# Kernel optimization log

Measured on AMD Instinct MI355X. Metric: run time of the kernel, lower is better.

## Reference

```python
import jax, jax.numpy as jnp
import numpy as np

B, T, D, K = 8, 4096, 1024, 3


def setup_inputs() -> dict:
    key = jax.random.key(0)
    k0, k1, k2 = jax.random.split(key, 3)
    x = jax.random.normal(k0, (B, T, D), dtype=jnp.float32)
    lim = 1.0 / np.sqrt(D)
    Wv = jax.random.uniform(k1, (D, D), dtype=jnp.float32, minval=-lim, maxval=lim)
    bv = jnp.zeros((D,), dtype=jnp.float32)
    Wo = jax.random.uniform(k2, (D, D), dtype=jnp.float32, minval=-lim, maxval=lim)
    bo = jnp.zeros((D,), dtype=jnp.float32)
    neighbor_weights = jnp.ones((K,), dtype=jnp.float32) / K
    return {"x": x, "Wv": Wv, "bv": bv, "Wo": Wo, "bo": bo,
            "neighbor_weights": neighbor_weights}


def reference(x, Wv, bv, Wo, bo, neighbor_weights):
    # x: [B, T, D]; faithful translation of the unfold -> Linear -> weighted-sum chain
    k = neighbor_weights.shape[0]
    pad = k // 2
    t = x.shape[1]
    # replicate padding along T (torch F.pad mode='replicate')
    xp = jnp.pad(x, ((0, 0), (pad, pad), (0, 0)), mode='edge')  # [B, T+2*pad, D]
    # sliding windows: [B, T, K, D] (small fixed K loop, not a data-dim loop)
    windows = jnp.stack([xp[:, i:i + t, :] for i in range(k)], axis=2)
    # value projection applied per window element (nn.Linear: x @ W.T + b)
    v = jnp.einsum('btkd,ed->btke', windows, Wv) + bv  # [B, T, K, D]
    # fixed-weight neighbor average
    attended = jnp.einsum('btkd,k->btd', v, neighbor_weights)  # [B, T, D]
    # output projection
    return jnp.einsum('btd,ed->bte', attended, Wo) + bo
```

## Files before the change

kernel.cpp:

```cpp
#include <hip/hip_runtime.h>
#include <stdint.h>
#include <stddef.h>

typedef _Float16 f16_t;
typedef _Float16 f16x4 __attribute__((ext_vector_type(4)));
typedef _Float16 f16x8 __attribute__((ext_vector_type(8)));
typedef float f32x4 __attribute__((ext_vector_type(4)));

#define AS_G __attribute__((address_space(1)))
#define AS_L __attribute__((address_space(3)))

__device__ __forceinline__ void gload_lds16(const void* g, void* l) {
  __builtin_amdgcn_global_load_lds((AS_G void*)g, (AS_L void*)l, 16, 0, 0);
}

#define FENCE() asm volatile("" ::: "memory")
#define BARX()                            \
  do {                                    \
    FENCE();                              \
    __builtin_amdgcn_s_barrier();         \
    FENCE();                              \
  } while (0)
#define VMCNT(n) asm volatile("s_waitcnt vmcnt(" #n ")" ::: "memory")


__global__ void cvt_f16_kernel(const float* __restrict__ in, f16_t* __restrict__ out, int n4) {
  int i = blockIdx.x * blockDim.x + threadIdx.x;
  if (i >= n4) return;
  f32x4 v = ((const f32x4*)in)[i];
  f16x4 o;
  o.x = (f16_t)v.x; o.y = (f16_t)v.y; o.z = (f16_t)v.z; o.w = (f16_t)v.w;
  ((f16x4*)out)[i] = o;
}

__global__ void transpose_cvt_kernel(const float* __restrict__ in, f16_t* __restrict__ out) {
  __shared__ float tile[32][33];
  const int bx = blockIdx.x, by = blockIdx.y;
  const int tx = threadIdx.x, ty = threadIdx.y;
#pragma unroll
  for (int i = 0; i < 32; i += 8)
    tile[ty + i][tx] = in[(size_t)(by * 32 + ty + i) * 1024 + bx * 32 + tx];
  __syncthreads();
#pragma unroll
  for (int i = 0; i < 32; i += 8)
    out[(size_t)(bx * 32 + ty + i) * 1024 + by * 32 + tx] = (f16_t)tile[tx][ty + i];
}

__global__ void bconst_kernel(const float* __restrict__ Wo, const float* __restrict__ bv,
                              const float* __restrict__ bo, const float* __restrict__ nw,
                              int Kw, float* __restrict__ bc) {
  const int e = blockIdx.x;
  const int t = threadIdx.x;
  float sw = 0.f;
  for (int k = 0; k < Kw; ++k) sw += nw[k];
  float p = 0.f;
  for (int d = t; d < 1024; d += 256) p += Wo[(size_t)e * 1024 + d] * bv[d];
  __shared__ float red[256];
  red[t] = p;
  __syncthreads();
  for (int s = 128; s > 0; s >>= 1) {
    if (t < s) red[t] += red[t + s];
    __syncthreads();
  }
  if (t == 0) bc[e] = sw * red[0] + bo[e];
}

__global__ void xavg_kernel(const float* __restrict__ x, const float* __restrict__ nw,
                            f16_t* __restrict__ out) {
  const int T = 4096, D = 1024;
  const int base = blockIdx.x * 8;
  const int t0 = base & (T - 1);
  const int col = threadIdx.x * 4;
  const float w0 = nw[0], w1 = nw[1], w2 = nw[2];
  const float* xb = x + (size_t)base * D + col;
  f32x4 a = *(const f32x4*)(xb + (t0 == 0 ? 0 : -D));
  f32x4 b = *(const f32x4*)(xb);
  f16_t* ob = out + (size_t)base * D + col;
#pragma unroll
  for (int g = 0; g < 8; ++g) {
    f32x4 c;
    if (t0 + g == T - 1) c = b;
    else c = *(const f32x4*)(xb + (size_t)(g + 1) * D);
    f32x4 y = w0 * a + w1 * b + w2 * c;
    f16x4 o;
    o.x = (f16_t)y.x; o.y = (f16_t)y.y; o.z = (f16_t)y.z; o.w = (f16_t)y.w;
    *(f16x4*)(ob + (size_t)g * D) = o;
    a = b;
    b = c;
  }
}


template <typename OutT, bool BIAS>
__global__ __launch_bounds__(256) void gemm_bt_kernel(const f16_t* __restrict__ A,
                                                      const f16_t* __restrict__ Bt,
                                                      OutT* __restrict__ C,
                                                      const float* __restrict__ bias,
                                                      int M, int N, int K) {
  __shared__ __align__(16) f16_t sA[128 * 32];
  __shared__ __align__(16) f16_t sB[128 * 32];
  const int tid = threadIdx.x;
  const int l = tid & 63;
  const int w = tid >> 6;
  const int wr = w >> 1;
  const int wc = w & 1;
  const int nMT = M >> 7;
  const int bid = blockIdx.x;
  const int mt = bid % nMT;
  const int nt = bid / nMT;
  const int m0 = mt << 7;
  const int n0 = nt << 7;

  const int srow = (w << 4) + (l >> 2);
  const int scol = (l & 3) << 3;
  const size_t aoff0 = (size_t)(m0 + srow) * K + scol;
  const size_t boff0 = (size_t)(n0 + srow) * K + scol;
  f16_t* ldsA = sA + (w << 9);
  f16_t* ldsB = sB + (w << 9);

  f32x4 acc[4][4];
#pragma unroll
  for (int i = 0; i < 4; ++i)
#pragma unroll
    for (int j = 0; j < 4; ++j) acc[i][j] = f32x4{0.f, 0.f, 0.f, 0.f};

  const int ka = (l >> 4) << 3;
  const int ar = (wr << 6) + (l & 15);
  const int br = (wc << 6) + (l & 15);

  const int nK = K >> 5;
  for (int kt = 0; kt < nK; ++kt) {
    const int kb = kt << 5;
    gload_lds16(A + aoff0 + kb, ldsA);
    gload_lds16(A + aoff0 + ((size_t)K << 6) + kb, ldsA + 2048);
    gload_lds16(Bt + boff0 + kb, ldsB);
    gload_lds16(Bt + boff0 + ((size_t)K << 6) + kb, ldsB + 2048);
    __syncthreads();
    f16x8 af[4], bfr[4];
#pragma unroll
    for (int m = 0; m < 4; ++m) af[m] = *(const f16x8*)(sA + ((ar + (m << 4)) << 5) + ka);
#pragma unroll
    for (int n = 0; n < 4; ++n) bfr[n] = *(const f16x8*)(sB + ((br + (n << 4)) << 5) + ka);
#pragma unroll
    for (int m = 0; m < 4; ++m)
#pragma unroll
      for (int n = 0; n < 4; ++n)
        acc[m][n] = __builtin_amdgcn_mfma_f32_16x16x32_f16(af[m], bfr[n], acc[m][n], 0, 0, 0);
    __syncthreads();
  }

  const int orow = (l >> 4) << 2;
  const int ocol = l & 15;
#pragma unroll
  for (int n = 0; n < 4; ++n) {
    const int gn = n0 + (wc << 6) + (n << 4) + ocol;
    const float bs = BIAS ? bias[gn] : 0.f;
#pragma unroll
    for (int m = 0; m < 4; ++m) {
      const int gm = m0 + (wr << 6) + (m << 4) + orow;
#pragma unroll
      for (int j = 0; j < 4; ++j) {
        C[(size_t)(gm + j) * N + gn] = (OutT)(acc[m][n][j] + bs);
      }
    }
  }
}


__device__ __forceinline__ void stage256(const f16_t* __restrict__ g, int K,
                                         f16_t* ldsOp, int w, int l) {
#pragma unroll
  for (int i = 0; i < 2; ++i) {
    const int f = i * 512 + w * 64 + l;
    const int row = f >> 2;
    const int ch = f & 3;
    const int col = ((ch ^ ((row >> 1) & 3)) << 3);
    gload_lds16(g + (size_t)row * K + col, ldsOp + i * 4096 + w * 512);
  }
}

__global__ __launch_bounds__(512, 2) void gemm256_kernel(const f16_t* __restrict__ A,
                                                         const f16_t* __restrict__ Bt,
                                                         float* __restrict__ C,
                                                         const float* __restrict__ bias,
                                                         int M, int N, int K) {
  __shared__ __align__(16) f16_t lds[4 * 16384];
  const int tid = threadIdx.x;
  const int l = tid & 63;
  const int w = tid >> 6;
  const int wr = w >> 2;
  const int wc = w & 3;

  const int nwg = gridDim.x;
  const int cpx = nwg >> 3;
  const int swz = (blockIdx.x & 7) * cpx + (blockIdx.x >> 3);
  const int nNT = N >> 8;
  const int mt = swz / nNT;
  const int nt = swz % nNT;
  const int m0 = mt << 8;
  const int n0 = nt << 8;

  const f16_t* Apanel = A + (size_t)m0 * K;
  const f16_t* Bpanel = Bt + (size_t)n0 * K;

  const int lr = l & 15;
  const int q = l >> 4;
  const int sw = ((q ^ ((lr >> 1) & 3)) << 3);

  f32x4 acc[8][4];
#pragma unroll
  for (int m = 0; m < 8; ++m)
#pragma unroll
    for (int n = 0; n < 4; ++n) acc[m][n] = f32x4{0.f, 0.f, 0.f, 0.f};

  const int nK = K >> 5;

  for (int t = 0; t < 3; ++t) {
    f16_t* buf = lds + (t & 3) * 16384;
    stage256(Apanel + (t << 5), K, buf, w, l);
    stage256(Bpanel + (t << 5), K, buf + 8192, w, l);
  }
  VMCNT(8);
  BARX();

  for (int t = 0; t < nK; ++t) {
    f16_t* sA = lds + (t & 3) * 16384;
    f16_t* sB = sA + 8192;

    f16x8 bf[4], af[4];
#pragma unroll
    for (int n = 0; n < 4; ++n)
      bf[n] = *(const f16x8*)(sB + (((wc << 6) + (n << 4) + lr) << 5) + sw);
#pragma unroll
    for (int m = 0; m < 4; ++m)
      af[m] = *(const f16x8*)(sA + (((wr << 7) + (m << 4) + lr) << 5) + sw);
    if (t + 3 < nK) {
      f16_t* nbuf = lds + ((t + 3) & 3) * 16384;
      stage256(Apanel + ((size_t)(t + 3) << 5), K, nbuf, w, l);
    }
    BARX();
    __builtin_amdgcn_s_setprio(1);
#pragma unroll
    for (int m = 0; m < 4; ++m)
#pragma unroll
      for (int n = 0; n < 4; ++n)
        acc[m][n] = __builtin_amdgcn_mfma_f32_16x16x32_f16(af[m], bf[n], acc[m][n], 0, 0, 0);
    __builtin_amdgcn_s_setprio(0);
    BARX();

    f16x8 ag[4];
#pragma unroll
    for (int m = 0; m < 4; ++m)
      ag[m] = *(const f16x8*)(sA + (((wr << 7) + 64 + (m << 4) + lr) << 5) + sw);
    if (t + 3 < nK) {
      f16_t* nbuf = lds + ((t + 3) & 3) * 16384;
      stage256(Bpanel + ((size_t)(t + 3) << 5), K, nbuf + 8192, w, l);
    }
    BARX();
    __builtin_amdgcn_s_setprio(1);
#pragma unroll
    for (int m = 0; m < 4; ++m)
#pragma unroll
      for (int n = 0; n < 4; ++n)
        acc[m + 4][n] = __builtin_amdgcn_mfma_f32_16x16x32_f16(ag[m], bf[n], acc[m + 4][n], 0, 0, 0);
    __builtin_amdgcn_s_setprio(0);
    VMCNT(8);
    BARX();
  }

  float bs[4];
#pragma unroll
  for (int n = 0; n < 4; ++n) bs[n] = bias[n0 + (wc << 6) + (n << 4) + lr];
#pragma unroll
  for (int m = 0; m < 8; ++m) {
    const int gm = m0 + (wr << 7) + (m << 4) + (q << 2);
#pragma unroll
    for (int j = 0; j < 4; ++j) {
      float* Crow = C + (size_t)(gm + j) * N + n0 + (wc << 6) + lr;
#pragma unroll
      for (int n = 0; n < 4; ++n) Crow[n << 4] = acc[m][n][j] + bs[n];
    }
  }
}


extern "C" void kernel_launch(void* const* d_in, const int* in_sizes, int n_in,
                              void* d_out, int out_size, void* d_ws, size_t ws_size,
                              hipStream_t stream) {
  const float* x = (const float*)d_in[0];
  const float* Wv = (const float*)d_in[1];
  const float* bv = (const float*)d_in[2];
  const float* Wo = (const float*)d_in[3];
  const float* bo = (const float*)d_in[4];
  const float* nw = (const float*)d_in[5];
  float* out = (float*)d_out;

  char* ws = (char*)d_ws;
  f16_t* Wo_h = (f16_t*)(ws);
  f16_t* WvT  = (f16_t*)(ws + (2u << 20));
  f16_t* WcT  = (f16_t*)(ws + (4u << 20));
  float* bc   = (float*)(ws + (6u << 20));
  f16_t* Xavg = (f16_t*)(ws + (8u << 20));

  cvt_f16_kernel<<<dim3(1024), dim3(256), 0, stream>>>(Wo, Wo_h, 1024 * 1024 / 4);
  transpose_cvt_kernel<<<dim3(32, 32), dim3(32, 8), 0, stream>>>(Wv, WvT);
  bconst_kernel<<<dim3(1024), dim3(256), 0, stream>>>(Wo, bv, bo, nw, in_sizes[5], bc);
  xavg_kernel<<<dim3(32768 / 8), dim3(256), 0, stream>>>(x, nw, Xavg);
  gemm_bt_kernel<f16_t, false><<<dim3(64), dim3(256), 0, stream>>>(
      Wo_h, WvT, WcT, (const float*)nullptr, 1024, 1024, 1024);
  gemm256_kernel<<<dim3(512), dim3(512), 0, stream>>>(
      Xavg, WcT, out, bc, 32768, 1024, 1024);
}
```

Baseline: 158.7 us.

## Fuse neighbor-averaging of x into the main GEMM A-tile loading

Removes the separate xavg kernel that wrote an averaged fp16 copy of x, and instead loads fp32 x rows directly in the main GEMM, computes the 3-tap weighted average in registers, converts to fp16 and writes it into a padded LDS A tile. B staging becomes a 3-stage ring while A is double-buffered through registers. The intent is to avoid the 64MB fp16 intermediate write and read-back. In exchange the GEMM reads fp32 x with roughly 2x row redundancy (4 rows per 2 outputs) through plain vector loads, and the pipeline depth for A shrinks.

Measured after the change: 155.2 us. 1.02x faster.

```diff
diff --git a/kernel.cpp b/kernel.cpp
--- a/kernel.cpp
+++ b/kernel.cpp
@@ -22,6 +22,7 @@
     FENCE();                              \
   } while (0)
 #define VMCNT(n) asm volatile("s_waitcnt vmcnt(" #n ")" ::: "memory")
+#define LGKM0() asm volatile("s_waitcnt lgkmcnt(0)" ::: "memory")
 
 
 __global__ void cvt_f16_kernel(const float* __restrict__ in, f16_t* __restrict__ out, int n4) {
@@ -63,31 +64,6 @@
     __syncthreads();
   }
   if (t == 0) bc[e] = sw * red[0] + bo[e];
-}
-
-__global__ void xavg_kernel(const float* __restrict__ x, const float* __restrict__ nw,
-                            f16_t* __restrict__ out) {
-  const int T = 4096, D = 1024;
-  const int base = blockIdx.x * 8;
-  const int t0 = base & (T - 1);
-  const int col = threadIdx.x * 4;
-  const float w0 = nw[0], w1 = nw[1], w2 = nw[2];
-  const float* xb = x + (size_t)base * D + col;
-  f32x4 a = *(const f32x4*)(xb + (t0 == 0 ? 0 : -D));
-  f32x4 b = *(const f32x4*)(xb);
-  f16_t* ob = out + (size_t)base * D + col;
-#pragma unroll
-  for (int g = 0; g < 8; ++g) {
-    f32x4 c;
-    if (t0 + g == T - 1) c = b;
-    else c = *(const f32x4*)(xb + (size_t)(g + 1) * D);
-    f32x4 y = w0 * a + w1 * b + w2 * c;
-    f16x4 o;
-    o.x = (f16_t)y.x; o.y = (f16_t)y.y; o.z = (f16_t)y.z; o.w = (f16_t)y.w;
-    *(f16x4*)(ob + (size_t)g * D) = o;
-    a = b;
-    b = c;
-  }
 }
 
 
@@ -167,8 +143,8 @@
 }
 
 
-__device__ __forceinline__ void stage256(const f16_t* __restrict__ g, int K,
-                                         f16_t* ldsOp, int w, int l) {
+__device__ __forceinline__ void stageB(const f16_t* __restrict__ g, int K,
+                                       f16_t* ldsOp, int w, int l) {
 #pragma unroll
   for (int i = 0; i < 2; ++i) {
     const int f = i * 512 + w * 64 + l;
@@ -179,33 +155,77 @@
   }
 }
 
-__global__ __launch_bounds__(512, 2) void gemm256_kernel(const f16_t* __restrict__ A,
-                                                         const f16_t* __restrict__ Bt,
-                                                         float* __restrict__ C,
-                                                         const float* __restrict__ bias,
-                                                         int M, int N, int K) {
-  __shared__ __align__(16) f16_t lds[4 * 16384];
+__global__ __launch_bounds__(512, 2) void gemm_fused_kernel(
+    const float* __restrict__ X, const f16_t* __restrict__ Bt,
+    float* __restrict__ C, const float* __restrict__ bias,
+    const float* __restrict__ nw) {
+  constexpr int N = 1024, K = 1024, T = 4096;
+  constexpr int nK = K >> 5;
+  constexpr int AST = 40;
+  __shared__ __align__(16) f16_t sA[2 * 256 * AST];
+  __shared__ __align__(16) f16_t sB[3 * 8192];
+
   const int tid = threadIdx.x;
   const int l = tid & 63;
   const int w = tid >> 6;
   const int wr = w >> 2;
   const int wc = w & 3;
-
-  const int nwg = gridDim.x;
-  const int cpx = nwg >> 3;
-  const int swz = (blockIdx.x & 7) * cpx + (blockIdx.x >> 3);
+  const int lr = l & 15;
+  const int q = l >> 4;
+
+  const int cpx = (int)gridDim.x >> 3;
+  const int swz = ((int)blockIdx.x & 7) * cpx + ((int)blockIdx.x >> 3);
   const int nNT = N >> 8;
   const int mt = swz / nNT;
   const int nt = swz % nNT;
   const int m0 = mt << 8;
   const int n0 = nt << 8;
 
-  const f16_t* Apanel = A + (size_t)m0 * K;
   const f16_t* Bpanel = Bt + (size_t)n0 * K;
 
-  const int lr = l & 15;
-  const int q = l >> 4;
-  const int sw = ((q ^ ((lr >> 1) & 3)) << 3);
+  const int rp = tid >> 2;
+  const int cch = tid & 3;
+  const bool bst = (m0 & (T - 1)) == 0;
+  const bool ben = ((m0 + 256) & (T - 1)) == 0;
+  const int r0 = rp << 1, r1 = r0 + 1;
+  const int rm = (rp == 0 && bst) ? 0 : r0 - 1;
+  const int r2 = (rp == 127 && ben) ? r1 : r1 + 1;
+  const float* pxm = X + (size_t)(m0 + rm) * K + (cch << 3);
+  const float* px0 = X + (size_t)(m0 + r0) * K + (cch << 3);
+  const float* px1 = X + (size_t)(m0 + r1) * K + (cch << 3);
+  const float* px2 = X + (size_t)(m0 + r2) * K + (cch << 3);
+  const float w0 = nw[0], w1 = nw[1], w2 = nw[2];
+
+  f32x4 va0, va1, vb0, vb1, vc0, vc1, vd0, vd1;
+
+#define ALOAD(kt)                                          \
+  do {                                                     \
+    const int off_ = (kt) << 5;                            \
+    va0 = *(const f32x4*)(pxm + off_);                     \
+    va1 = *(const f32x4*)(pxm + off_ + 4);                 \
+    vb0 = *(const f32x4*)(px0 + off_);                     \
+    vb1 = *(const f32x4*)(px0 + off_ + 4);                 \
+    vc0 = *(const f32x4*)(px1 + off_);                     \
+    vc1 = *(const f32x4*)(px1 + off_ + 4);                 \
+    vd0 = *(const f32x4*)(px2 + off_);                     \
+    vd1 = *(const f32x4*)(px2 + off_ + 4);                 \
+  } while (0)
+
+#define AWRITE(buf)                                                      \
+  do {                                                                   \
+    f16_t* dst_ = sA + (buf) * (256 * AST);                              \
+    f32x4 t00 = w0 * va0 + w1 * vb0 + w2 * vc0;                          \
+    f32x4 t01 = w0 * va1 + w1 * vb1 + w2 * vc1;                          \
+    f32x4 t10 = w0 * vb0 + w1 * vc0 + w2 * vd0;                          \
+    f32x4 t11 = w0 * vb1 + w1 * vc1 + w2 * vd1;                          \
+    f16x8 y0_, y1_;                                                      \
+    _Pragma("unroll") for (int e = 0; e < 4; ++e) {                      \
+      y0_[e] = (f16_t)t00[e]; y0_[e + 4] = (f16_t)t01[e];                \
+      y1_[e] = (f16_t)t10[e]; y1_[e + 4] = (f16_t)t11[e];                \
+    }                                                                    \
+    *(f16x8*)(dst_ + r0 * AST + (cch << 3)) = y0_;                       \
+    *(f16x8*)(dst_ + r1 * AST + (cch << 3)) = y1_;                       \
+  } while (0)
 
   f32x4 acc[8][4];
 #pragma unroll
@@ -213,31 +233,30 @@
 #pragma unroll
     for (int n = 0; n < 4; ++n) acc[m][n] = f32x4{0.f, 0.f, 0.f, 0.f};
 
-  const int nK = K >> 5;
-
-  for (int t = 0; t < 3; ++t) {
-    f16_t* buf = lds + (t & 3) * 16384;
-    stage256(Apanel + (t << 5), K, buf, w, l);
-    stage256(Bpanel + (t << 5), K, buf + 8192, w, l);
-  }
-  VMCNT(8);
+  const int swB = (q ^ ((lr >> 1) & 3)) << 3;
+
+  ALOAD(0);
+  stageB(Bpanel, K, sB, w, l);
+  stageB(Bpanel + 32, K, sB + 8192, w, l);
+  VMCNT(4);
+  AWRITE(0);
+  ALOAD(1);
+  VMCNT(10);
+  LGKM0();
   BARX();
 
   for (int t = 0; t < nK; ++t) {
-    f16_t* sA = lds + (t & 3) * 16384;
-    f16_t* sB = sA + 8192;
+    f16_t* cA = sA + (t & 1) * (256 * AST);
+    f16_t* cB = sB + (t % 3) * 8192;
 
     f16x8 bf[4], af[4];
 #pragma unroll
     for (int n = 0; n < 4; ++n)
-      bf[n] = *(const f16x8*)(sB + (((wc << 6) + (n << 4) + lr) << 5) + sw);
-#pragma unroll
-    for (int m = 0; m < 4; ++m)
-      af[m] = *(const f16x8*)(sA + (((wr << 7) + (m << 4) + lr) << 5) + sw);
-    if (t + 3 < nK) {
-      f16_t* nbuf = lds + ((t + 3) & 3) * 16384;
-      stage256(Apanel + ((size_t)(t + 3) << 5), K, nbuf, w, l);
-    }
+      bf[n] = *(const f16x8*)(cB + (((wc << 6) + (n << 4) + lr) << 5) + swB);
+#pragma unroll
+    for (int m = 0; m < 4; ++m)
+      af[m] = *(const f16x8*)(cA + ((wr << 7) + (m << 4) + lr) * AST + (q << 3));
+    if (t + 2 < nK) stageB(Bpanel + ((t + 2) << 5), K, sB + ((t + 2) % 3) * 8192, w, l);
     BARX();
     __builtin_amdgcn_s_setprio(1);
 #pragma unroll
@@ -251,11 +270,10 @@
     f16x8 ag[4];
 #pragma unroll
     for (int m = 0; m < 4; ++m)
-      ag[m] = *(const f16x8*)(sA + (((wr << 7) + 64 + (m << 4) + lr) << 5) + sw);
-    if (t + 3 < nK) {
-      f16_t* nbuf = lds + ((t + 3) & 3) * 16384;
-      stage256(Bpanel + ((size_t)(t + 3) << 5), K, nbuf + 8192, w, l);
-    }
+      ag[m] = *(const f16x8*)(cA + ((wr << 7) + 64 + (m << 4) + lr) * AST + (q << 3));
+    VMCNT(2);
+    if (t + 1 < nK) AWRITE((t + 1) & 1);
+    if (t + 2 < nK) ALOAD(t + 2);
     BARX();
     __builtin_amdgcn_s_setprio(1);
 #pragma unroll
@@ -264,7 +282,7 @@
       for (int n = 0; n < 4; ++n)
         acc[m + 4][n] = __builtin_amdgcn_mfma_f32_16x16x32_f16(ag[m], bf[n], acc[m + 4][n], 0, 0, 0);
     __builtin_amdgcn_s_setprio(0);
-    VMCNT(8);
+    LGKM0();
     BARX();
   }
 
@@ -281,6 +299,8 @@
       for (int n = 0; n < 4; ++n) Crow[n << 4] = acc[m][n][j] + bs[n];
     }
   }
+#undef ALOAD
+#undef AWRITE
 }
 
 
@@ -300,14 +320,11 @@
   f16_t* WvT  = (f16_t*)(ws + (2u << 20));
   f16_t* WcT  = (f16_t*)(ws + (4u << 20));
   float* bc   = (float*)(ws + (6u << 20));
-  f16_t* Xavg = (f16_t*)(ws + (8u << 20));
 
   cvt_f16_kernel<<<dim3(1024), dim3(256), 0, stream>>>(Wo, Wo_h, 1024 * 1024 / 4);
   transpose_cvt_kernel<<<dim3(32, 32), dim3(32, 8), 0, stream>>>(Wv, WvT);
   bconst_kernel<<<dim3(1024), dim3(256), 0, stream>>>(Wo, bv, bo, nw, in_sizes[5], bc);
-  xavg_kernel<<<dim3(32768 / 8), dim3(256), 0, stream>>>(x, nw, Xavg);
   gemm_bt_kernel<f16_t, false><<<dim3(64), dim3(256), 0, stream>>>(
       Wo_h, WvT, WcT, (const float*)nullptr, 1024, 1024, 1024);
-  gemm256_kernel<<<dim3(512), dim3(512), 0, stream>>>(
-      Xavg, WcT, out, bc, 32768, 1024, 1024);
-}
+  gemm_fused_kernel<<<dim3(512), dim3(512), 0, stream>>>(x, WcT, out, bc, nw);
+}
```

## Merge prep kernels into one launch and cut GEMM main-loop barriers to one

Applied to the files above, without the earlier changes.

The four preprocessing kernels (Wo conversion, Wv transpose-convert, bias constant, neighbour-averaged X) are merged into one kernel that picks its job from the block index. This saves launch overhead and lets the small jobs run alongside the large X pass. In the 256x256 GEMM, each iteration now stages both the A and B tiles up front, loads all A/B fragments at once, and runs both MFMA halves back to back. That drops the per-iteration barrier count from four to one. In exchange, more fragment registers are live at once, and the final iterations issue redundant prefetch loads because the tile index is clamped rather than guarded.

Measured after the change: 146.8 us. -7.5%, faster.

```diff
diff --git a/kernel.cpp b/kernel.cpp
--- a/kernel.cpp
+++ b/kernel.cpp
@@ -24,69 +24,67 @@
 #define VMCNT(n) asm volatile("s_waitcnt vmcnt(" #n ")" ::: "memory")
 
 
-__global__ void cvt_f16_kernel(const float* __restrict__ in, f16_t* __restrict__ out, int n4) {
-  int i = blockIdx.x * blockDim.x + threadIdx.x;
-  if (i >= n4) return;
-  f32x4 v = ((const f32x4*)in)[i];
-  f16x4 o;
-  o.x = (f16_t)v.x; o.y = (f16_t)v.y; o.z = (f16_t)v.z; o.w = (f16_t)v.w;
-  ((f16x4*)out)[i] = o;
-}
-
-__global__ void transpose_cvt_kernel(const float* __restrict__ in, f16_t* __restrict__ out) {
-  __shared__ float tile[32][33];
-  const int bx = blockIdx.x, by = blockIdx.y;
-  const int tx = threadIdx.x, ty = threadIdx.y;
-#pragma unroll
-  for (int i = 0; i < 32; i += 8)
-    tile[ty + i][tx] = in[(size_t)(by * 32 + ty + i) * 1024 + bx * 32 + tx];
-  __syncthreads();
-#pragma unroll
-  for (int i = 0; i < 32; i += 8)
-    out[(size_t)(bx * 32 + ty + i) * 1024 + by * 32 + tx] = (f16_t)tile[tx][ty + i];
-}
-
-__global__ void bconst_kernel(const float* __restrict__ Wo, const float* __restrict__ bv,
-                              const float* __restrict__ bo, const float* __restrict__ nw,
-                              int Kw, float* __restrict__ bc) {
-  const int e = blockIdx.x;
+__global__ __launch_bounds__(256) void prep_xavg_kernel(
+    const float* __restrict__ X, const float* __restrict__ Wo,
+    const float* __restrict__ Wv, const float* __restrict__ bv,
+    const float* __restrict__ bo, const float* __restrict__ nw, int Kw,
+    f16_t* __restrict__ Wo_h, f16_t* __restrict__ WvT, float* __restrict__ bc,
+    f16_t* __restrict__ Xavg) {
+  __shared__ float smem[32 * 33];
+  const int b = blockIdx.x;
   const int t = threadIdx.x;
-  float sw = 0.f;
-  for (int k = 0; k < Kw; ++k) sw += nw[k];
-  float p = 0.f;
-  for (int d = t; d < 1024; d += 256) p += Wo[(size_t)e * 1024 + d] * bv[d];
-  __shared__ float red[256];
-  red[t] = p;
-  __syncthreads();
-  for (int s = 128; s > 0; s >>= 1) {
-    if (t < s) red[t] += red[t + s];
+  if (b >= 3072) {
+    const int T = 4096, D = 1024;
+    const int base = (b - 3072) * 8;
+    const int t0 = base & (T - 1);
+    const int col = t * 4;
+    const float w0 = nw[0], w1 = nw[1], w2 = nw[2];
+    const float* xb = X + (size_t)base * D + col;
+    f32x4 va = *(const f32x4*)(xb + (t0 == 0 ? 0 : -D));
+    f32x4 vb = *(const f32x4*)(xb);
+    f16_t* ob = Xavg + (size_t)base * D + col;
+#pragma unroll
+    for (int g = 0; g < 8; ++g) {
+      f32x4 vc;
+      if (t0 + g == T - 1) vc = vb;
+      else vc = *(const f32x4*)(xb + (size_t)(g + 1) * D);
+      f32x4 y = w0 * va + w1 * vb + w2 * vc;
+      f16x4 o;
+      o.x = (f16_t)y.x; o.y = (f16_t)y.y; o.z = (f16_t)y.z; o.w = (f16_t)y.w;
+      *(f16x4*)(ob + (size_t)g * D) = o;
+      va = vb;
+      vb = vc;
+    }
+  } else if (b < 1024) {
+    const int i = b * 256 + t;
+    f32x4 v = ((const f32x4*)Wo)[i];
+    f16x4 o;
+    o.x = (f16_t)v.x; o.y = (f16_t)v.y; o.z = (f16_t)v.z; o.w = (f16_t)v.w;
+    ((f16x4*)Wo_h)[i] = o;
+  } else if (b < 2048) {
+    const int i = b - 1024;
+    const int bx = i & 31, by = i >> 5;
+    const int tx = t & 31, ty = t >> 5;
+#pragma unroll
+    for (int k = 0; k < 32; k += 8)
+      smem[(ty + k) * 33 + tx] = Wv[(size_t)(by * 32 + ty + k) * 1024 + bx * 32 + tx];
     __syncthreads();
-  }
-  if (t == 0) bc[e] = sw * red[0] + bo[e];
-}
-
-__global__ void xavg_kernel(const float* __restrict__ x, const float* __restrict__ nw,
-                            f16_t* __restrict__ out) {
-  const int T = 4096, D = 1024;
-  const int base = blockIdx.x * 8;
-  const int t0 = base & (T - 1);
-  const int col = threadIdx.x * 4;
-  const float w0 = nw[0], w1 = nw[1], w2 = nw[2];
-  const float* xb = x + (size_t)base * D + col;
-  f32x4 a = *(const f32x4*)(xb + (t0 == 0 ? 0 : -D));
-  f32x4 b = *(const f32x4*)(xb);
-  f16_t* ob = out + (size_t)base * D + col;
-#pragma unroll
-  for (int g = 0; g < 8; ++g) {
-    f32x4 c;
-    if (t0 + g == T - 1) c = b;
-    else c = *(const f32x4*)(xb + (size_t)(g + 1) * D);
-    f32x4 y = w0 * a + w1 * b + w2 * c;
-    f16x4 o;
-    o.x = (f16_t)y.x; o.y = (f16_t)y.y; o.z = (f16_t)y.z; o.w = (f16_t)y.w;
-    *(f16x4*)(ob + (size_t)g * D) = o;
-    a = b;
-    b = c;
+#pragma unroll
+    for (int k = 0; k < 32; k += 8)
+      WvT[(size_t)(bx * 32 + ty + k) * 1024 + by * 32 + tx] = (f16_t)smem[tx * 33 + ty + k];
+  } else {
+    const int e = b - 2048;
+    float sw = 0.f;
+    for (int k = 0; k < Kw; ++k) sw += nw[k];
+    float p = 0.f;
+    for (int d = t; d < 1024; d += 256) p += Wo[(size_t)e * 1024 + d] * bv[d];
+    smem[t] = p;
+    __syncthreads();
+    for (int s = 128; s > 0; s >>= 1) {
+      if (t < s) smem[t] += smem[t + s];
+      __syncthreads();
+    }
+    if (t == 0) bc[e] = sw * smem[0] + bo[e];
   }
 }
 
@@ -190,22 +188,20 @@
   const int w = tid >> 6;
   const int wr = w >> 2;
   const int wc = w & 3;
-
-  const int nwg = gridDim.x;
-  const int cpx = nwg >> 3;
-  const int swz = (blockIdx.x & 7) * cpx + (blockIdx.x >> 3);
+  const int lr = l & 15;
+  const int q = l >> 4;
+
+  const int cpx = (int)gridDim.x >> 3;
+  const int swzb = ((int)blockIdx.x & 7) * cpx + ((int)blockIdx.x >> 3);
   const int nNT = N >> 8;
-  const int mt = swz / nNT;
-  const int nt = swz % nNT;
+  const int mt = swzb / nNT;
+  const int nt = swzb % nNT;
   const int m0 = mt << 8;
   const int n0 = nt << 8;
 
   const f16_t* Apanel = A + (size_t)m0 * K;
   const f16_t* Bpanel = Bt + (size_t)n0 * K;
-
-  const int lr = l & 15;
-  const int q = l >> 4;
-  const int sw = ((q ^ ((lr >> 1) & 3)) << 3);
+  const int sw = (q ^ ((lr >> 1) & 3)) << 3;
 
   f32x4 acc[8][4];
 #pragma unroll
@@ -227,43 +223,37 @@
     f16_t* sA = lds + (t & 3) * 16384;
     f16_t* sB = sA + 8192;
 
-    f16x8 bf[4], af[4];
+    {
+      const int tn = (t + 3) < nK ? (t + 3) : (nK - 1);
+      f16_t* nbuf = lds + ((t + 3) & 3) * 16384;
+      stage256(Apanel + ((size_t)tn << 5), K, nbuf, w, l);
+      stage256(Bpanel + ((size_t)tn << 5), K, nbuf + 8192, w, l);
+    }
+
+    f16x8 bf[4], af[4], ag[4];
 #pragma unroll
     for (int n = 0; n < 4; ++n)
       bf[n] = *(const f16x8*)(sB + (((wc << 6) + (n << 4) + lr) << 5) + sw);
 #pragma unroll
     for (int m = 0; m < 4; ++m)
       af[m] = *(const f16x8*)(sA + (((wr << 7) + (m << 4) + lr) << 5) + sw);
-    if (t + 3 < nK) {
-      f16_t* nbuf = lds + ((t + 3) & 3) * 16384;
-      stage256(Apanel + ((size_t)(t + 3) << 5), K, nbuf, w, l);
-    }
-    BARX();
+#pragma unroll
+    for (int m = 0; m < 4; ++m)
+      ag[m] = *(const f16x8*)(sA + (((wr << 7) + 64 + (m << 4) + lr) << 5) + sw);
+
     __builtin_amdgcn_s_setprio(1);
 #pragma unroll
     for (int m = 0; m < 4; ++m)
 #pragma unroll
       for (int n = 0; n < 4; ++n)
         acc[m][n] = __builtin_amdgcn_mfma_f32_16x16x32_f16(af[m], bf[n], acc[m][n], 0, 0, 0);
-    __builtin_amdgcn_s_setprio(0);
-    BARX();
-
-    f16x8 ag[4];
-#pragma unroll
-    for (int m = 0; m < 4; ++m)
-      ag[m] = *(const f16x8*)(sA + (((wr << 7) + 64 + (m << 4) + lr) << 5) + sw);
-    if (t + 3 < nK) {
-      f16_t* nbuf = lds + ((t + 3) & 3) * 16384;
-      stage256(Bpanel + ((size_t)(t + 3) << 5), K, nbuf + 8192, w, l);
-    }
-    BARX();
-    __builtin_amdgcn_s_setprio(1);
 #pragma unroll
     for (int m = 0; m < 4; ++m)
 #pragma unroll
       for (int n = 0; n < 4; ++n)
         acc[m + 4][n] = __builtin_amdgcn_mfma_f32_16x16x32_f16(ag[m], bf[n], acc[m + 4][n], 0, 0, 0);
     __builtin_amdgcn_s_setprio(0);
+
     VMCNT(8);
     BARX();
   }
@@ -302,10 +292,8 @@
   float* bc   = (float*)(ws + (6u << 20));
   f16_t* Xavg = (f16_t*)(ws + (8u << 20));
 
-  cvt_f16_kernel<<<dim3(1024), dim3(256), 0, stream>>>(Wo, Wo_h, 1024 * 1024 / 4);
-  transpose_cvt_kernel<<<dim3(32, 32), dim3(32, 8), 0, stream>>>(Wv, WvT);
-  bconst_kernel<<<dim3(1024), dim3(256), 0, stream>>>(Wo, bv, bo, nw, in_sizes[5], bc);
-  xavg_kernel<<<dim3(32768 / 8), dim3(256), 0, stream>>>(x, nw, Xavg);
+  prep_xavg_kernel<<<dim3(7168), dim3(256), 0, stream>>>(
+      x, Wo, Wv, bv, bo, nw, in_sizes[5], Wo_h, WvT, bc, Xavg);
   gemm_bt_kernel<f16_t, false><<<dim3(64), dim3(256), 0, stream>>>(
       Wo_h, WvT, WcT, (const float*)nullptr, 1024, 1024, 1024);
   gemm256_kernel<<<dim3(512), dim3(512), 0, stream>>>(
```
